# Kernel tuning notes

Hardware: AMD Instinct MI355X
Metric: run time of the kernel (lower is better)

The kernel has to match this reference:

```python
import jax, jax.numpy as jnp
import numpy as np

TH = 1.0  # LIF threshold
EPS = 1e-5  # LayerNorm eps

# Heaviside spike with snntorch ATan surrogate gradient (alpha=2.0)
@jax.custom_vjp
def spike(u):
    return (u > 0).astype(u.dtype)

def _spike_fwd(u):
    return spike(u), u

def _spike_bwd(u, g):
    alpha = 2.0
    return (g * (alpha / 2.0) / (1.0 + (jnp.pi / 2.0 * alpha * u) ** 2),)

spike.defvjp(_spike_fwd, _spike_bwd)


def setup_inputs() -> dict:
    key = jax.random.key(0)
    ks = jax.random.split(key, 8)
    T, B, D_in, H1, H2, D_lat = 200, 256, 256, 512, 512, 128
    spike_input = jax.random.uniform(ks[0], (T, B, D_in), dtype=jnp.float32)
    s1 = 1.0 / np.sqrt(D_in)
    s2 = 1.0 / np.sqrt(H1)
    s3 = 1.0 / np.sqrt(H2)
    return {
        "spike_input": spike_input,
        "W1": jax.random.uniform(ks[1], (H1, D_in), jnp.float32, -s1, s1),
        "b1": jnp.zeros((H1,), jnp.float32),
        "beta0": jnp.float32(0.5),
        "W2": jax.random.uniform(ks[2], (H2, H1), jnp.float32, -s2, s2),
        "b2": jnp.zeros((H2,), jnp.float32),
        "beta1": jnp.float32(0.5),
        "Wout": jax.random.uniform(ks[3], (D_lat, H2), jnp.float32, -s3, s3),
        "bout": jnp.zeros((D_lat,), jnp.float32),
        "ln_gamma": jnp.ones((D_lat,), jnp.float32),
        "ln_beta": jnp.zeros((D_lat,), jnp.float32),
    }


def reference(spike_input, W1, b1, beta0, W2, b2, beta1, Wout, bout, ln_gamma, ln_beta):
    T, B, _ = spike_input.shape
    H1, H2 = W1.shape[0], W2.shape[0]
    be0 = jnp.clip(beta0, 0.0, 1.0)
    be1 = jnp.clip(beta1, 0.0, 1.0)

    def step(carry, x_t):
        m0, m1 = carry
        # layer 0: Linear + Leaky (reset-by-subtraction, reset detached)
        h = x_t @ W1.T + b1
        r0 = jax.lax.stop_gradient((m0 > TH).astype(h.dtype))
        m0 = be0 * m0 + h - r0 * TH
        s0 = spike(m0 - TH)
        # layer 1
        h2 = s0 @ W2.T + b2
        r1 = jax.lax.stop_gradient((m1 > TH).astype(h2.dtype))
        m1 = be1 * m1 + h2 - r1 * TH
        s1 = spike(m1 - TH)
        return (m0, m1), (s0, s1)

    init = (jnp.zeros((B, H1), spike_input.dtype), jnp.zeros((B, H2), spike_input.dtype))
    _, (spk0, spk1) = jax.lax.scan(step, init, spike_input)  # [T,B,H]

    # source appends only the final-timestep activation to hidden_acc
    hidden_mean = spk1[-1]  # [B, H2]
    latent = hidden_mean @ Wout.T + bout
    mu = jnp.mean(latent, axis=-1, keepdims=True)
    var = jnp.var(latent, axis=-1, keepdims=True)
    latent = (latent - mu) * jax.lax.rsqrt(var + EPS) * ln_gamma + ln_beta

    fr0 = jnp.mean(spk0, axis=0)
    fr1 = jnp.mean(spk1, axis=0)
    return latent, fr0, fr1
```

## Files before the change

kernel.cpp:

```cpp
#include <hip/hip_runtime.h>

typedef _Float16 half8 __attribute__((ext_vector_type(8)));
typedef _Float16 half4v __attribute__((ext_vector_type(4)));
typedef float f32x4 __attribute__((ext_vector_type(4)));

#define T_STEPS 200
#define BATCH 256
#define D_IN 256
#define H1N 512
#define H2N 512
#define D_LAT 128
#define BHE (BATCH * H1N)
#define TC 100
#define NCH 2
#define MC (TC * BATCH)

__global__ __launch_bounds__(256) void split_kern(const float* __restrict__ in,
                                                  _Float16* __restrict__ hi,
                                                  _Float16* __restrict__ lo, int n4) {
    int i = blockIdx.x * 256 + threadIdx.x;
    if (i >= n4) return;
    float4 v = reinterpret_cast<const float4*>(in)[i];
    float vv[4] = {v.x, v.y, v.z, v.w};
    half4v h, l;
#pragma unroll
    for (int c = 0; c < 4; ++c) {
        _Float16 hh = (_Float16)vv[c];
        h[c] = hh;
        l[c] = (_Float16)((vv[c] - (float)hh) * 2048.0f);
    }
    reinterpret_cast<half4v*>(hi)[i] = h;
    reinterpret_cast<half4v*>(lo)[i] = l;
}

template <bool ASPLIT>
__global__ __launch_bounds__(256, 2) void gemm_mfma(const _Float16* __restrict__ Ah,
                                                    const _Float16* __restrict__ Al,
                                                    const _Float16* __restrict__ Bh,
                                                    const _Float16* __restrict__ Bl,
                                                    const float* __restrict__ bias,
                                                    float* __restrict__ C,
                                                    int M, int N, int K) {
    __shared__ _Float16 sAh[128 * 32];
    __shared__ _Float16 sAl[128 * 32];
    __shared__ _Float16 sBh[128 * 32];
    __shared__ _Float16 sBl[128 * 32];

    const int tid = threadIdx.x;
    const int lane = tid & 63, wid = tid >> 6;
    const int wr = wid >> 1, wc = wid & 1;
    const int m0 = blockIdx.x * 128, n0 = blockIdx.y * 128;
    const int frow = lane & 15, kb = lane >> 4;
    const int swf = (frow >> 1) & 3;

    const int srow = tid >> 2;
    const int ls = tid & 3;

    f32x4 acc0[4][4] = {};
    f32x4 acc1[4][4] = {};

    for (int k0 = 0; k0 < K; k0 += 32) {
#pragma unroll
        for (int c = 0; c < 2; ++c) {
            const int row = c * 64 + srow;
            const int sw = (row >> 1) & 3;
            const int dst = row * 32 + 8 * (ls ^ sw);
            const size_t asrc = (size_t)(m0 + row) * K + k0 + 8 * ls;
            const size_t bsrc = (size_t)(n0 + row) * K + k0 + 8 * ls;
            *reinterpret_cast<uint4*>(&sAh[dst]) = *reinterpret_cast<const uint4*>(&Ah[asrc]);
            if constexpr (ASPLIT)
                *reinterpret_cast<uint4*>(&sAl[dst]) = *reinterpret_cast<const uint4*>(&Al[asrc]);
            *reinterpret_cast<uint4*>(&sBh[dst]) = *reinterpret_cast<const uint4*>(&Bh[bsrc]);
            *reinterpret_cast<uint4*>(&sBl[dst]) = *reinterpret_cast<const uint4*>(&Bl[bsrc]);
        }
        __syncthreads();

        half8 ah[4], al[4];
#pragma unroll
        for (int mi = 0; mi < 4; ++mi) {
            const int off = (wr * 64 + mi * 16 + frow) * 32 + 8 * (kb ^ swf);
            ah[mi] = *reinterpret_cast<const half8*>(&sAh[off]);
            if constexpr (ASPLIT) al[mi] = *reinterpret_cast<const half8*>(&sAl[off]);
        }
#pragma unroll
        for (int ni = 0; ni < 4; ++ni) {
            const int off = (wc * 64 + ni * 16 + frow) * 32 + 8 * (kb ^ swf);
            half8 bh = *reinterpret_cast<const half8*>(&sBh[off]);
            half8 bl = *reinterpret_cast<const half8*>(&sBl[off]);
#pragma unroll
            for (int mi = 0; mi < 4; ++mi) {
                acc0[mi][ni] = __builtin_amdgcn_mfma_f32_16x16x32_f16(ah[mi], bh, acc0[mi][ni], 0, 0, 0);
                acc1[mi][ni] = __builtin_amdgcn_mfma_f32_16x16x32_f16(ah[mi], bl, acc1[mi][ni], 0, 0, 0);
                if constexpr (ASPLIT)
                    acc1[mi][ni] = __builtin_amdgcn_mfma_f32_16x16x32_f16(al[mi], bh, acc1[mi][ni], 0, 0, 0);
            }
        }
        __syncthreads();
    }

#pragma unroll
    for (int mi = 0; mi < 4; ++mi) {
#pragma unroll
        for (int ni = 0; ni < 4; ++ni) {
            const int col = n0 + wc * 64 + ni * 16 + frow;
            const float bb = bias[col];
#pragma unroll
            for (int r = 0; r < 4; ++r) {
                const int m = m0 + wr * 64 + mi * 16 + kb * 4 + r;
                C[(size_t)m * N + col] =
                    acc0[mi][ni][r] + 4.8828125e-4f * acc1[mi][ni][r] + bb;
            }
        }
    }
}

__global__ __launch_bounds__(256) void lif_scan_c(const float* __restrict__ H,
                                                  const float* __restrict__ beta_ptr,
                                                  _Float16* __restrict__ S,
                                                  float* __restrict__ m_state,
                                                  float* __restrict__ cnt_state,
                                                  float* __restrict__ fr_out,
                                                  unsigned char* __restrict__ s_last,
                                                  int first, int last, int writeS, int writeLast) {
    const int idx = blockIdx.x * 256 + threadIdx.x;
    const float be = fminf(fmaxf(beta_ptr[0], 0.f), 1.f);
    float m = first ? 0.f : m_state[idx];
    float cnt = first ? 0.f : cnt_state[idx];
    float r = (m > 1.0f) ? 1.f : 0.f;
#pragma unroll 4
    for (int t = 0; t < TC; ++t) {
        const float h = H[(size_t)t * BHE + idx];
        m = be * m + h - r;
        const bool sp = m > 1.0f;
        r = sp ? 1.f : 0.f;
        cnt += sp ? 1.f : 0.f;
        if (writeS) S[(size_t)t * BHE + idx] = sp ? (_Float16)1.f : (_Float16)0.f;
    }
    if (last) {
        fr_out[idx] = cnt / 200.0f;
        if (writeLast) s_last[idx] = (r > 0.5f) ? 1 : 0;
    } else {
        m_state[idx] = m;
        cnt_state[idx] = cnt;
    }
}

__global__ __launch_bounds__(128) void latent_ln(const unsigned char* __restrict__ s_last,
                                                 const float* __restrict__ Wout,
                                                 const float* __restrict__ bout,
                                                 const float* __restrict__ gamma,
                                                 const float* __restrict__ lbeta,
                                                 float* __restrict__ out) {
    const int b = blockIdx.x;
    const int d = threadIdx.x;
    __shared__ float sv[H2N];
    for (int k = d; k < H2N; k += 128) sv[k] = (float)s_last[b * H2N + k];
    __syncthreads();

    float a = 0.f;
    const float* w = &Wout[(size_t)d * H2N];
#pragma unroll 8
    for (int k = 0; k < H2N; ++k) a = fmaf(sv[k], w[k], a);
    a += bout[d];

    __shared__ float red[128];
    red[d] = a;
    __syncthreads();
    for (int s = 64; s > 0; s >>= 1) {
        if (d < s) red[d] += red[d + s];
        __syncthreads();
    }
    const float mu = red[0] * (1.0f / 128.0f);
    __syncthreads();
    const float df = a - mu;
    red[d] = df * df;
    __syncthreads();
    for (int s = 64; s > 0; s >>= 1) {
        if (d < s) red[d] += red[d + s];
        __syncthreads();
    }
    const float var = red[0] * (1.0f / 128.0f);
    out[(size_t)b * D_LAT + d] = df * (1.0f / sqrtf(var + 1e-5f)) * gamma[d] + lbeta[d];
}

extern "C" void kernel_launch(void* const* d_in, const int* in_sizes, int n_in,
                              void* d_out, int out_size, void* d_ws, size_t ws_size,
                              hipStream_t stream) {
    const float* X     = (const float*)d_in[0];
    const float* W1    = (const float*)d_in[1];
    const float* b1    = (const float*)d_in[2];
    const float* beta0 = (const float*)d_in[3];
    const float* W2    = (const float*)d_in[4];
    const float* b2    = (const float*)d_in[5];
    const float* beta1 = (const float*)d_in[6];
    const float* Wout  = (const float*)d_in[7];
    const float* bout  = (const float*)d_in[8];
    const float* lng   = (const float*)d_in[9];
    const float* lnb   = (const float*)d_in[10];

    float* out    = (float*)d_out;
    float* latent = out;
    float* fr0    = out + BATCH * D_LAT;
    float* fr1    = fr0 + BATCH * H1N;

    char* p = (char*)d_ws;
    float*     H_c = (float*)p;               p += (size_t)MC * H1N * 4;
    _Float16*  Xh  = (_Float16*)p;            p += (size_t)MC * D_IN * 2;
    _Float16*  Xl  = (_Float16*)p;            p += (size_t)MC * D_IN * 2;
    _Float16*  S0  = (_Float16*)p;            p += (size_t)MC * H1N * 2;
    _Float16*  W1h = (_Float16*)p;            p += (size_t)H1N * D_IN * 2;
    _Float16*  W1l = (_Float16*)p;            p += (size_t)H1N * D_IN * 2;
    _Float16*  W2h = (_Float16*)p;            p += (size_t)H2N * H1N * 2;
    _Float16*  W2l = (_Float16*)p;            p += (size_t)H2N * H1N * 2;
    float*     m0s = (float*)p;               p += (size_t)BHE * 4;
    float*     c0s = (float*)p;               p += (size_t)BHE * 4;
    float*     m1s = (float*)p;               p += (size_t)BHE * 4;
    float*     c1s = (float*)p;               p += (size_t)BHE * 4;
    unsigned char* s1l = (unsigned char*)p;   p += (size_t)BHE;

    split_kern<<<dim3((H1N * D_IN / 4 + 255) / 256), 256, 0, stream>>>(W1, W1h, W1l, H1N * D_IN / 4);
    split_kern<<<dim3((H2N * H1N / 4 + 255) / 256), 256, 0, stream>>>(W2, W2h, W2l, H2N * H1N / 4);

    for (int c = 0; c < NCH; ++c) {
        const float* Xc = X + (size_t)c * TC * BATCH * D_IN;
        const int first = (c == 0), last = (c == NCH - 1);
        split_kern<<<dim3((MC * D_IN / 4 + 255) / 256), 256, 0, stream>>>(Xc, Xh, Xl, MC * D_IN / 4);
        gemm_mfma<true><<<dim3(MC / 128, H1N / 128), 256, 0, stream>>>(
            Xh, Xl, W1h, W1l, b1, H_c, MC, H1N, D_IN);
        lif_scan_c<<<dim3(BHE / 256), 256, 0, stream>>>(
            H_c, beta0, S0, m0s, c0s, fr0, nullptr, first, last, 1, 0);
        gemm_mfma<false><<<dim3(MC / 128, H2N / 128), 256, 0, stream>>>(
            S0, nullptr, W2h, W2l, b2, H_c, MC, H2N, H1N);
        lif_scan_c<<<dim3(BHE / 256), 256, 0, stream>>>(
            H_c, beta1, nullptr, m1s, c1s, fr1, s1l, first, last, 0, 1);
    }
    latent_ln<<<dim3(BATCH), 128, 0, stream>>>(s1l, Wout, bout, lng, lnb, latent);
}
```

Baseline: 406.3 us.

## Fuse input split into GEMM1, add async LDS double-buffering, vectorize LIF scan

Removes the separate fp16 hi/lo split pass over the input by converting X tiles on the fly inside the first GEMM. Both GEMMs now use 64x128 tiles with 512 threads, double-buffered LDS filled through global_load_lds. The LIF scan handles four neurons per thread with float4 loads. The time chunks shrink from 100 to 50 steps, and the two weight splits are merged into one launch. The LIF kernel now launches only 256 blocks of 128 threads, which limits parallelism in that serial stage, and there are twice as many chunk launches.

```diff
diff --git a/kernel.cpp b/kernel.cpp
--- a/kernel.cpp
+++ b/kernel.cpp
@@ -1,7 +1,7 @@
 #include <hip/hip_runtime.h>
 
 typedef _Float16 half8 __attribute__((ext_vector_type(8)));
-typedef _Float16 half4v __attribute__((ext_vector_type(4)));
+typedef _Float16 half4 __attribute__((ext_vector_type(4)));
 typedef float f32x4 __attribute__((ext_vector_type(4)));
 
 #define T_STEPS 200
@@ -11,138 +11,262 @@
 #define H2N 512
 #define D_LAT 128
 #define BHE (BATCH * H1N)
-#define TC 100
-#define NCH 2
+#define TC 50
+#define NCH 4
 #define MC (TC * BATCH)
-
-__global__ __launch_bounds__(256) void split_kern(const float* __restrict__ in,
-                                                  _Float16* __restrict__ hi,
-                                                  _Float16* __restrict__ lo, int n4) {
-    int i = blockIdx.x * 256 + threadIdx.x;
-    if (i >= n4) return;
-    float4 v = reinterpret_cast<const float4*>(in)[i];
+#define SC_LO 4.8828125e-4f
+
+struct alignas(8) H4 { _Float16 v[4]; };
+struct alignas(4) U4 { unsigned char v[4]; };
+
+__device__ __forceinline__ void glds16(const void* g, void* l) {
+    __builtin_amdgcn_global_load_lds(
+        (const __attribute__((address_space(1))) unsigned int*)g,
+        (__attribute__((address_space(3))) unsigned int*)l, 16, 0, 0);
+}
+
+__global__ __launch_bounds__(512, 4) void gemm2_k(const _Float16* __restrict__ A,
+                                                  const _Float16* __restrict__ Bh,
+                                                  const _Float16* __restrict__ Bl,
+                                                  const float* __restrict__ bias,
+                                                  float* __restrict__ C,
+                                                  int M, int N, int K) {
+    __shared__ _Float16 sA[2][64 * 32];
+    __shared__ _Float16 sBh[2][128 * 32];
+    __shared__ _Float16 sBl[2][128 * 32];
+
+    const int tid = threadIdx.x, lane = tid & 63, wid = tid >> 6;
+    const int m0 = blockIdx.x * 64, n0 = blockIdx.y * 128;
+    const int wr = wid >> 2, wc = wid & 3;
+    const int frow = lane & 15, kb = lane >> 4;
+    const int srow16 = lane >> 2, sls = lane & 3;
+
+    f32x4 acc0[2][2] = {};
+    f32x4 acc1[2][2] = {};
+    const int nk = K / 32;
+
+    auto stage = [&](int ph, int k0) {
+        for (int j = wid; j < 20; j += 8) {
+            const _Float16* gb;
+            _Float16* lb;
+            int row0;
+            if (j < 4)       { gb = A  + (size_t)m0 * K; lb = &sA[ph][0];  row0 = j * 16; }
+            else if (j < 12) { gb = Bh + (size_t)n0 * K; lb = &sBh[ph][0]; row0 = (j - 4) * 16; }
+            else             { gb = Bl + (size_t)n0 * K; lb = &sBl[ph][0]; row0 = (j - 12) * 16; }
+            const int row = row0 + srow16;
+            const int gs = sls ^ ((row >> 1) & 3);
+            glds16(gb + (size_t)row * K + k0 + 8 * gs, lb + row0 * 32);
+        }
+    };
+
+    stage(0, 0);
+    __syncthreads();
+
+    for (int kt = 0; kt < nk; ++kt) {
+        const int ph = kt & 1;
+        if (kt + 1 < nk) stage(ph ^ 1, (kt + 1) * 32);
+
+        half8 bh[2], bl[2];
+#pragma unroll
+        for (int ni = 0; ni < 2; ++ni) {
+            const int br = wc * 32 + ni * 16 + frow;
+            const int off = br * 32 + 8 * (kb ^ ((br >> 1) & 3));
+            bh[ni] = *reinterpret_cast<const half8*>(&sBh[ph][off]);
+            bl[ni] = *reinterpret_cast<const half8*>(&sBl[ph][off]);
+        }
+#pragma unroll
+        for (int mi = 0; mi < 2; ++mi) {
+            const int ar = wr * 32 + mi * 16 + frow;
+            half8 a = *reinterpret_cast<const half8*>(&sA[ph][ar * 32 + 8 * (kb ^ ((ar >> 1) & 3))]);
+#pragma unroll
+            for (int ni = 0; ni < 2; ++ni) {
+                acc0[mi][ni] = __builtin_amdgcn_mfma_f32_16x16x32_f16(a, bh[ni], acc0[mi][ni], 0, 0, 0);
+                acc1[mi][ni] = __builtin_amdgcn_mfma_f32_16x16x32_f16(a, bl[ni], acc1[mi][ni], 0, 0, 0);
+            }
+        }
+        __syncthreads();
+    }
+
+#pragma unroll
+    for (int mi = 0; mi < 2; ++mi)
+#pragma unroll
+        for (int ni = 0; ni < 2; ++ni) {
+            const int col = n0 + wc * 32 + ni * 16 + frow;
+            const float bb = bias[col];
+#pragma unroll
+            for (int r = 0; r < 4; ++r) {
+                const int m = m0 + wr * 32 + mi * 16 + kb * 4 + r;
+                C[(size_t)m * N + col] = acc0[mi][ni][r] + SC_LO * acc1[mi][ni][r] + bb;
+            }
+        }
+}
+
+__global__ __launch_bounds__(512, 4) void gemm1_k(const float* __restrict__ X,
+                                                  const _Float16* __restrict__ Bh,
+                                                  const _Float16* __restrict__ Bl,
+                                                  const float* __restrict__ bias,
+                                                  float* __restrict__ C,
+                                                  int M, int N, int K) {
+    __shared__ _Float16 sAh[2][64 * 32];
+    __shared__ _Float16 sAl[2][64 * 32];
+    __shared__ _Float16 sBh[2][128 * 32];
+    __shared__ _Float16 sBl[2][128 * 32];
+
+    const int tid = threadIdx.x, lane = tid & 63, wid = tid >> 6;
+    const int m0 = blockIdx.x * 64, n0 = blockIdx.y * 128;
+    const int wr = wid >> 2, wc = wid & 3;
+    const int frow = lane & 15, kb = lane >> 4;
+    const int srow16 = lane >> 2, sls = lane & 3;
+    const int arow = tid >> 3, aq = tid & 7;
+
+    f32x4 acc0[2][2] = {};
+    f32x4 acc1[2][2] = {};
+    const int nk = K / 32;
+
+    auto stageB = [&](int ph, int k0) {
+        for (int j = wid; j < 16; j += 8) {
+            const _Float16* gb = (j < 8) ? Bh : Bl;
+            _Float16* lb = (j < 8) ? &sBh[ph][0] : &sBl[ph][0];
+            const int row0 = (j & 7) * 16;
+            const int row = row0 + srow16;
+            const int gs = sls ^ ((row >> 1) & 3);
+            glds16(gb + (size_t)(n0 + row) * K + k0 + 8 * gs, lb + row0 * 32);
+        }
+    };
+    auto stageA = [&](int ph, int k0) {
+        float4 v = *reinterpret_cast<const float4*>(&X[(size_t)(m0 + arow) * K + k0 + aq * 4]);
+        float vv[4] = {v.x, v.y, v.z, v.w};
+        half4 h, l;
+#pragma unroll
+        for (int c = 0; c < 4; ++c) {
+            _Float16 hh = (_Float16)vv[c];
+            h[c] = hh;
+            l[c] = (_Float16)((vv[c] - (float)hh) * 2048.0f);
+        }
+        const int off = arow * 32 + 8 * ((aq >> 1) ^ ((arow >> 1) & 3)) + 4 * (aq & 1);
+        *reinterpret_cast<half4*>(&sAh[ph][off]) = h;
+        *reinterpret_cast<half4*>(&sAl[ph][off]) = l;
+    };
+
+    stageB(0, 0);
+    stageA(0, 0);
+    __syncthreads();
+
+    for (int kt = 0; kt < nk; ++kt) {
+        const int ph = kt & 1;
+        if (kt + 1 < nk) {
+            stageB(ph ^ 1, (kt + 1) * 32);
+            stageA(ph ^ 1, (kt + 1) * 32);
+        }
+        half8 bh[2], bl[2];
+#pragma unroll
+        for (int ni = 0; ni < 2; ++ni) {
+            const int br = wc * 32 + ni * 16 + frow;
+            const int off = br * 32 + 8 * (kb ^ ((br >> 1) & 3));
+            bh[ni] = *reinterpret_cast<const half8*>(&sBh[ph][off]);
+            bl[ni] = *reinterpret_cast<const half8*>(&sBl[ph][off]);
+        }
+#pragma unroll
+        for (int mi = 0; mi < 2; ++mi) {
+            const int ar = wr * 32 + mi * 16 + frow;
+            const int aoff = ar * 32 + 8 * (kb ^ ((ar >> 1) & 3));
+            half8 ah = *reinterpret_cast<const half8*>(&sAh[ph][aoff]);
+            half8 al = *reinterpret_cast<const half8*>(&sAl[ph][aoff]);
+#pragma unroll
+            for (int ni = 0; ni < 2; ++ni) {
+                acc0[mi][ni] = __builtin_amdgcn_mfma_f32_16x16x32_f16(ah, bh[ni], acc0[mi][ni], 0, 0, 0);
+                acc1[mi][ni] = __builtin_amdgcn_mfma_f32_16x16x32_f16(ah, bl[ni], acc1[mi][ni], 0, 0, 0);
+                acc1[mi][ni] = __builtin_amdgcn_mfma_f32_16x16x32_f16(al, bh[ni], acc1[mi][ni], 0, 0, 0);
+            }
+        }
+        __syncthreads();
+    }
+
+#pragma unroll
+    for (int mi = 0; mi < 2; ++mi)
+#pragma unroll
+        for (int ni = 0; ni < 2; ++ni) {
+            const int col = n0 + wc * 32 + ni * 16 + frow;
+            const float bb = bias[col];
+#pragma unroll
+            for (int r = 0; r < 4; ++r) {
+                const int m = m0 + wr * 32 + mi * 16 + kb * 4 + r;
+                C[(size_t)m * N + col] = acc0[mi][ni][r] + SC_LO * acc1[mi][ni][r] + bb;
+            }
+        }
+}
+
+__global__ __launch_bounds__(128) void lif4(const float4* __restrict__ H,
+                                            const float* __restrict__ beta_ptr,
+                                            H4* __restrict__ S,
+                                            float4* __restrict__ mst,
+                                            float4* __restrict__ cst,
+                                            float4* __restrict__ fr,
+                                            U4* __restrict__ slast,
+                                            int first, int last, int writeS, int writeLast) {
+    const int idx = blockIdx.x * 128 + threadIdx.x;
+    const float be = fminf(fmaxf(beta_ptr[0], 0.f), 1.f);
+    float m[4], cnt[4], r[4];
+    if (first) {
+#pragma unroll
+        for (int c = 0; c < 4; ++c) { m[c] = 0.f; cnt[c] = 0.f; r[c] = 0.f; }
+    } else {
+        float4 mv = mst[idx], cv = cst[idx];
+        m[0] = mv.x; m[1] = mv.y; m[2] = mv.z; m[3] = mv.w;
+        cnt[0] = cv.x; cnt[1] = cv.y; cnt[2] = cv.z; cnt[3] = cv.w;
+#pragma unroll
+        for (int c = 0; c < 4; ++c) r[c] = (m[c] > 1.0f) ? 1.f : 0.f;
+    }
+#pragma unroll 2
+    for (int t = 0; t < TC; ++t) {
+        float4 hv = H[(size_t)t * (BHE / 4) + idx];
+        float h[4] = {hv.x, hv.y, hv.z, hv.w};
+        H4 s;
+#pragma unroll
+        for (int c = 0; c < 4; ++c) {
+            m[c] = be * m[c] + h[c] - r[c];
+            const bool sp = m[c] > 1.0f;
+            r[c] = sp ? 1.f : 0.f;
+            cnt[c] += sp ? 1.f : 0.f;
+            s.v[c] = (_Float16)r[c];
+        }
+        if (writeS) S[(size_t)t * (BHE / 4) + idx] = s;
+    }
+    if (last) {
+        fr[idx] = make_float4(cnt[0] * (1.f / 200.f), cnt[1] * (1.f / 200.f),
+                              cnt[2] * (1.f / 200.f), cnt[3] * (1.f / 200.f));
+        if (writeLast) {
+            U4 u;
+#pragma unroll
+            for (int c = 0; c < 4; ++c) u.v[c] = (r[c] > 0.5f) ? 1 : 0;
+            slast[idx] = u;
+        }
+    } else {
+        mst[idx] = make_float4(m[0], m[1], m[2], m[3]);
+        cst[idx] = make_float4(cnt[0], cnt[1], cnt[2], cnt[3]);
+    }
+}
+
+__global__ __launch_bounds__(256) void wsplit(const float* __restrict__ W1, const float* __restrict__ W2,
+                                              _Float16* __restrict__ W1h, _Float16* __restrict__ W1l,
+                                              _Float16* __restrict__ W2h, _Float16* __restrict__ W2l) {
+    const int i = blockIdx.x * 256 + threadIdx.x;
+    const float* src;
+    _Float16 *dh, *dl;
+    int k;
+    if (i < 32768) { src = W1; dh = W1h; dl = W1l; k = i; }
+    else           { src = W2; dh = W2h; dl = W2l; k = i - 32768; }
+    float4 v = reinterpret_cast<const float4*>(src)[k];
     float vv[4] = {v.x, v.y, v.z, v.w};
-    half4v h, l;
+    half4 h, l;
 #pragma unroll
     for (int c = 0; c < 4; ++c) {
         _Float16 hh = (_Float16)vv[c];
         h[c] = hh;
         l[c] = (_Float16)((vv[c] - (float)hh) * 2048.0f);
     }
-    reinterpret_cast<half4v*>(hi)[i] = h;
-    reinterpret_cast<half4v*>(lo)[i] = l;
-}
-
-template <bool ASPLIT>
-__global__ __launch_bounds__(256, 2) void gemm_mfma(const _Float16* __restrict__ Ah,
-                                                    const _Float16* __restrict__ Al,
-                                                    const _Float16* __restrict__ Bh,
-                                                    const _Float16* __restrict__ Bl,
-                                                    const float* __restrict__ bias,
-                                                    float* __restrict__ C,
-                                                    int M, int N, int K) {
-    __shared__ _Float16 sAh[128 * 32];
-    __shared__ _Float16 sAl[128 * 32];
-    __shared__ _Float16 sBh[128 * 32];
-    __shared__ _Float16 sBl[128 * 32];
-
-    const int tid = threadIdx.x;
-    const int lane = tid & 63, wid = tid >> 6;
-    const int wr = wid >> 1, wc = wid & 1;
-    const int m0 = blockIdx.x * 128, n0 = blockIdx.y * 128;
-    const int frow = lane & 15, kb = lane >> 4;
-    const int swf = (frow >> 1) & 3;
-
-    const int srow = tid >> 2;
-    const int ls = tid & 3;
-
-    f32x4 acc0[4][4] = {};
-    f32x4 acc1[4][4] = {};
-
-    for (int k0 = 0; k0 < K; k0 += 32) {
-#pragma unroll
-        for (int c = 0; c < 2; ++c) {
-            const int row = c * 64 + srow;
-            const int sw = (row >> 1) & 3;
-            const int dst = row * 32 + 8 * (ls ^ sw);
-            const size_t asrc = (size_t)(m0 + row) * K + k0 + 8 * ls;
-            const size_t bsrc = (size_t)(n0 + row) * K + k0 + 8 * ls;
-            *reinterpret_cast<uint4*>(&sAh[dst]) = *reinterpret_cast<const uint4*>(&Ah[asrc]);
-            if constexpr (ASPLIT)
-                *reinterpret_cast<uint4*>(&sAl[dst]) = *reinterpret_cast<const uint4*>(&Al[asrc]);
-            *reinterpret_cast<uint4*>(&sBh[dst]) = *reinterpret_cast<const uint4*>(&Bh[bsrc]);
-            *reinterpret_cast<uint4*>(&sBl[dst]) = *reinterpret_cast<const uint4*>(&Bl[bsrc]);
-        }
-        __syncthreads();
-
-        half8 ah[4], al[4];
-#pragma unroll
-        for (int mi = 0; mi < 4; ++mi) {
-            const int off = (wr * 64 + mi * 16 + frow) * 32 + 8 * (kb ^ swf);
-            ah[mi] = *reinterpret_cast<const half8*>(&sAh[off]);
-            if constexpr (ASPLIT) al[mi] = *reinterpret_cast<const half8*>(&sAl[off]);
-        }
-#pragma unroll
-        for (int ni = 0; ni < 4; ++ni) {
-            const int off = (wc * 64 + ni * 16 + frow) * 32 + 8 * (kb ^ swf);
-            half8 bh = *reinterpret_cast<const half8*>(&sBh[off]);
-            half8 bl = *reinterpret_cast<const half8*>(&sBl[off]);
-#pragma unroll
-            for (int mi = 0; mi < 4; ++mi) {
-                acc0[mi][ni] = __builtin_amdgcn_mfma_f32_16x16x32_f16(ah[mi], bh, acc0[mi][ni], 0, 0, 0);
-                acc1[mi][ni] = __builtin_amdgcn_mfma_f32_16x16x32_f16(ah[mi], bl, acc1[mi][ni], 0, 0, 0);
-                if constexpr (ASPLIT)
-                    acc1[mi][ni] = __builtin_amdgcn_mfma_f32_16x16x32_f16(al[mi], bh, acc1[mi][ni], 0, 0, 0);
-            }
-        }
-        __syncthreads();
-    }
-
-#pragma unroll
-    for (int mi = 0; mi < 4; ++mi) {
-#pragma unroll
-        for (int ni = 0; ni < 4; ++ni) {
-            const int col = n0 + wc * 64 + ni * 16 + frow;
-            const float bb = bias[col];
-#pragma unroll
-            for (int r = 0; r < 4; ++r) {
-                const int m = m0 + wr * 64 + mi * 16 + kb * 4 + r;
-                C[(size_t)m * N + col] =
-                    acc0[mi][ni][r] + 4.8828125e-4f * acc1[mi][ni][r] + bb;
-            }
-        }
-    }
-}
-
-__global__ __launch_bounds__(256) void lif_scan_c(const float* __restrict__ H,
-                                                  const float* __restrict__ beta_ptr,
-                                                  _Float16* __restrict__ S,
-                                                  float* __restrict__ m_state,
-                                                  float* __restrict__ cnt_state,
-                                                  float* __restrict__ fr_out,
-                                                  unsigned char* __restrict__ s_last,
-                                                  int first, int last, int writeS, int writeLast) {
-    const int idx = blockIdx.x * 256 + threadIdx.x;
-    const float be = fminf(fmaxf(beta_ptr[0], 0.f), 1.f);
-    float m = first ? 0.f : m_state[idx];
-    float cnt = first ? 0.f : cnt_state[idx];
-    float r = (m > 1.0f) ? 1.f : 0.f;
-#pragma unroll 4
-    for (int t = 0; t < TC; ++t) {
-        const float h = H[(size_t)t * BHE + idx];
-        m = be * m + h - r;
-        const bool sp = m > 1.0f;
-        r = sp ? 1.f : 0.f;
-        cnt += sp ? 1.f : 0.f;
-        if (writeS) S[(size_t)t * BHE + idx] = sp ? (_Float16)1.f : (_Float16)0.f;
-    }
-    if (last) {
-        fr_out[idx] = cnt / 200.0f;
-        if (writeLast) s_last[idx] = (r > 0.5f) ? 1 : 0;
-    } else {
-        m_state[idx] = m;
-        cnt_state[idx] = cnt;
-    }
+    reinterpret_cast<half4*>(dh)[k] = h;
+    reinterpret_cast<half4*>(dl)[k] = l;
 }
 
 __global__ __launch_bounds__(128) void latent_ln(const unsigned char* __restrict__ s_last,
@@ -204,35 +328,33 @@
     float* fr1    = fr0 + BATCH * H1N;
 
     char* p = (char*)d_ws;
-    float*     H_c = (float*)p;               p += (size_t)MC * H1N * 4;
-    _Float16*  Xh  = (_Float16*)p;            p += (size_t)MC * D_IN * 2;
-    _Float16*  Xl  = (_Float16*)p;            p += (size_t)MC * D_IN * 2;
-    _Float16*  S0  = (_Float16*)p;            p += (size_t)MC * H1N * 2;
-    _Float16*  W1h = (_Float16*)p;            p += (size_t)H1N * D_IN * 2;
-    _Float16*  W1l = (_Float16*)p;            p += (size_t)H1N * D_IN * 2;
-    _Float16*  W2h = (_Float16*)p;            p += (size_t)H2N * H1N * 2;
-    _Float16*  W2l = (_Float16*)p;            p += (size_t)H2N * H1N * 2;
-    float*     m0s = (float*)p;               p += (size_t)BHE * 4;
-    float*     c0s = (float*)p;               p += (size_t)BHE * 4;
-    float*     m1s = (float*)p;               p += (size_t)BHE * 4;
-    float*     c1s = (float*)p;               p += (size_t)BHE * 4;
-    unsigned char* s1l = (unsigned char*)p;   p += (size_t)BHE;
-
-    split_kern<<<dim3((H1N * D_IN / 4 + 255) / 256), 256, 0, stream>>>(W1, W1h, W1l, H1N * D_IN / 4);
-    split_kern<<<dim3((H2N * H1N / 4 + 255) / 256), 256, 0, stream>>>(W2, W2h, W2l, H2N * H1N / 4);
+    float*     H_c = (float*)p;              p += (size_t)MC * H1N * 4;
+    _Float16*  S0  = (_Float16*)p;           p += (size_t)MC * H1N * 2;
+    _Float16*  W1h = (_Float16*)p;           p += (size_t)H1N * D_IN * 2;
+    _Float16*  W1l = (_Float16*)p;           p += (size_t)H1N * D_IN * 2;
+    _Float16*  W2h = (_Float16*)p;           p += (size_t)H2N * H1N * 2;
+    _Float16*  W2l = (_Float16*)p;           p += (size_t)H2N * H1N * 2;
+    float*     m0s = (float*)p;              p += (size_t)BHE * 4;
+    float*     c0s = (float*)p;              p += (size_t)BHE * 4;
+    float*     m1s = (float*)p;              p += (size_t)BHE * 4;
+    float*     c1s = (float*)p;              p += (size_t)BHE * 4;
+    unsigned char* s1l = (unsigned char*)p;  p += (size_t)BHE;
+
+    wsplit<<<dim3(384), 256, 0, stream>>>(W1, W2, W1h, W1l, W2h, W2l);
 
     for (int c = 0; c < NCH; ++c) {
         const float* Xc = X + (size_t)c * TC * BATCH * D_IN;
         const int first = (c == 0), last = (c == NCH - 1);
-        split_kern<<<dim3((MC * D_IN / 4 + 255) / 256), 256, 0, stream>>>(Xc, Xh, Xl, MC * D_IN / 4);
-        gemm_mfma<true><<<dim3(MC / 128, H1N / 128), 256, 0, stream>>>(
-            Xh, Xl, W1h, W1l, b1, H_c, MC, H1N, D_IN);
-        lif_scan_c<<<dim3(BHE / 256), 256, 0, stream>>>(
-            H_c, beta0, S0, m0s, c0s, fr0, nullptr, first, last, 1, 0);
-        gemm_mfma<false><<<dim3(MC / 128, H2N / 128), 256, 0, stream>>>(
-            S0, nullptr, W2h, W2l, b2, H_c, MC, H2N, H1N);
-        lif_scan_c<<<dim3(BHE / 256), 256, 0, stream>>>(
-            H_c, beta1, nullptr, m1s, c1s, fr1, s1l, first, last, 0, 1);
+        gemm1_k<<<dim3(MC / 64, H1N / 128), 512, 0, stream>>>(
+            Xc, W1h, W1l, b1, H_c, MC, H1N, D_IN);
+        lif4<<<dim3(256), 128, 0, stream>>>(
+            (const float4*)H_c, beta0, (H4*)S0, (float4*)m0s, (float4*)c0s,
+            (float4*)fr0, nullptr, first, last, 1, 0);
+        gemm2_k<<<dim3(MC / 64, H2N / 128), 512, 0, stream>>>(
+            S0, W2h, W2l, b2, H_c, MC, H2N, H1N);
+        lif4<<<dim3(256), 128, 0, stream>>>(
+            (const float4*)H_c, beta1, nullptr, (float4*)m1s, (float4*)c1s,
+            (float4*)fr1, (U4*)s1l, first, last, 0, 1);
     }
     latent_ln<<<dim3(BATCH), 128, 0, stream>>>(s1l, Wout, bout, lng, lnb, latent);
 }
```

After: 452.7 us. +11.4%, slower.
